# Optimization experiments

Hardware: AMD Instinct MI355X
Metric: run time of the kernel (lower is better)

## Reference

```python
import jax, jax.numpy as jnp
import numpy as np

B, T, C = 4, 1024, 1024
H, G = 16, 1            # n_head, n_query_groups
D = C // H              # head_dim = 64
E, K = 4, 1             # moe_num_experts, moe_k
FF = 4 * C              # ffn/expert hidden = 4096
EPS = 1e-5


def setup_inputs() -> dict:
    key = jax.random.key(0)
    ks = jax.random.split(key, 24)
    w = lambda k, shape: (jax.random.normal(k, shape, jnp.float32) * 0.02)
    return {
        "x": jax.random.normal(ks[0], (B, T, C), jnp.float32),
        # attention (torch Linear weights stored as [in, out])
        "wq": w(ks[1], (C, C)), "wk": w(ks[2], (C, C)), "wv": w(ks[3], (C, C)),
        "wo": w(ks[4], (C, C)), "bo": jnp.zeros((C,), jnp.float32),
        # feedforward
        "ff_w1": w(ks[5], (C, FF)), "ff_b1": jnp.zeros((FF,), jnp.float32),
        "ff_w2": w(ks[6], (FF, C)), "ff_b2": jnp.zeros((C,), jnp.float32),
        # MoE experts (stacked) + gate
        "exp_w1": w(ks[7], (E, C, FF)), "exp_b1": jnp.zeros((E, FF), jnp.float32),
        "exp_w2": w(ks[8], (E, FF, C)), "exp_b2": jnp.zeros((E, C), jnp.float32),
        "gate_w": w(ks[9], (C, E)), "gate_b": jnp.zeros((E,), jnp.float32),
        # layernorms
        "ln1_g": jnp.ones((C,), jnp.float32), "ln1_b": jnp.zeros((C,), jnp.float32),
        "ln2_g": jnp.ones((C,), jnp.float32), "ln2_b": jnp.zeros((C,), jnp.float32),
        "ln3_g": jnp.ones((C,), jnp.float32), "ln3_b": jnp.zeros((C,), jnp.float32),
    }


def _ln(x, g, b):
    m = x.mean(-1, keepdims=True)
    v = x.var(-1, keepdims=True)
    return (x - m) / jnp.sqrt(v + EPS) * g + b


def reference(x, wq, wk, wv, wo, bo, ff_w1, ff_b1, ff_w2, ff_b2,
              exp_w1, exp_b1, exp_w2, exp_b2, gate_w, gate_b,
              ln1_g, ln1_b, ln2_g, ln2_b, ln3_g, ln3_b):
    Hg = H // G
    # ---- grouped-query causal self-attention ----
    h = _ln(x, ln1_g, ln1_b)
    # [B,T,C] -> [B,G,Hg,T,D]
    q = (h @ wq).reshape(B, T, G, Hg, D).transpose(0, 2, 3, 1, 4)
    k = (h @ wk).reshape(B, T, G, Hg, D).transpose(0, 2, 3, 1, 4)
    v = (h @ wv).reshape(B, T, G, Hg, D).transpose(0, 2, 3, 1, 4)
    scores = jnp.einsum('bghtd,bghsd->bghts', q, k) / np.float32(np.sqrt(D))
    causal = jnp.tril(jnp.ones((T, T), bool))
    scores = jnp.where(causal, scores, -jnp.inf)
    probs = jax.nn.softmax(scores, axis=-1)
    o = jnp.einsum('bghts,bghsd->bghtd', probs, v)          # [B,G,Hg,T,D]
    o = o.reshape(B, H, T, D).transpose(0, 2, 1, 3).reshape(B, T, C)
    x = x + o @ wo + bo
    # ---- dense feedforward ----
    h = _ln(x, ln2_g, ln2_b)
    x = x + jax.nn.relu(h @ ff_w1 + ff_b1) @ ff_w2 + ff_b2
    # ---- MoE: compute ALL experts densely, gather top-k (faithful to source) ----
    h = _ln(x, ln3_g, ln3_b)
    gate = h @ gate_w + gate_b                               # [B,T,E]
    topk_s, topk_i = jax.lax.top_k(gate, K)                  # [B,T,K]
    topk_w = jax.nn.softmax(topk_s, axis=-1)
    hidden = jax.nn.relu(jnp.einsum('btc,ech->bteh', h, exp_w1) + exp_b1)
    expert_out = jnp.einsum('bteh,ehc->btec', hidden, exp_w2) + exp_b2  # [B,T,E,C]
    sel = jnp.take_along_axis(expert_out, topk_i[..., None], axis=2)    # [B,T,K,C]
    moe = (sel * topk_w[..., None]).sum(axis=2)
    return x + moe
```

## Files before the change

### kernel.cpp

```cpp
#include <hip/hip_runtime.h>


using f16   = _Float16;
using f16x4 = __attribute__((ext_vector_type(4))) _Float16;
using f16x8 = __attribute__((ext_vector_type(8))) _Float16;
using f32x4 = __attribute__((ext_vector_type(4))) float;

__device__ __forceinline__ void async16(void* l, const void* g) {
  __builtin_amdgcn_global_load_lds(
      (const __attribute__((address_space(1))) unsigned*)g,
      (__attribute__((address_space(3))) unsigned*)l, 16, 0, 0);
}

template <bool SPLITW>
__global__ __launch_bounds__(256) void transpose_k(
    const float* __restrict__ in, f16* __restrict__ oh, f16* __restrict__ ol,
    int R, int Cc) {
  __shared__ float tile[32][33];
  const int nbx = Cc >> 5;
  const int bx = blockIdx.x % nbx, by = blockIdx.x / nbx;
  const int tx = threadIdx.x & 31, ty = threadIdx.x >> 5;
#pragma unroll
  for (int i = 0; i < 4; ++i) {
    int r = ty + i * 8;
    tile[r][tx] = in[(size_t)(by * 32 + r) * Cc + bx * 32 + tx];
  }
  __syncthreads();
#pragma unroll
  for (int i = 0; i < 4; ++i) {
    int oc = ty + i * 8;
    float v = tile[tx][oc];
    size_t o = (size_t)(bx * 32 + oc) * R + by * 32 + tx;
    f16 hi = (f16)v;
    oh[o] = hi;
    if constexpr (SPLITW) ol[o] = (f16)(v - (float)hi);
  }
}

__global__ __launch_bounds__(256) void ln_k(
    const float* __restrict__ x, const float* __restrict__ g,
    const float* __restrict__ b, f16* __restrict__ outh, f16* __restrict__ outl) {
  const int row = blockIdx.x;
  const float4 vv = ((const float4*)(x + (size_t)row * 1024))[threadIdx.x];
  float s = vv.x + vv.y + vv.z + vv.w;
  float sq = vv.x * vv.x + vv.y * vv.y + vv.z * vv.z + vv.w * vv.w;
#pragma unroll
  for (int mm = 32; mm; mm >>= 1) { s += __shfl_xor(s, mm); sq += __shfl_xor(sq, mm); }
  __shared__ float red[8];
  const int wv = threadIdx.x >> 6;
  if ((threadIdx.x & 63) == 0) { red[wv] = s; red[4 + wv] = sq; }
  __syncthreads();
  s = red[0] + red[1] + red[2] + red[3];
  sq = red[4] + red[5] + red[6] + red[7];
  const float mean = s * 0.0009765625f;
  const float rstd = rsqrtf(sq * 0.0009765625f - mean * mean + 1e-5f);
  const int c = threadIdx.x * 4;
  const float xs[4] = {vv.x, vv.y, vv.z, vv.w};
  f16x4 ovh, ovl;
#pragma unroll
  for (int i = 0; i < 4; ++i) {
    float val = (xs[i] - mean) * rstd * g[c + i] + b[c + i];
    f16 hi = (f16)val;
    ovh[i] = hi;
    ovl[i] = (f16)(val - (float)hi);
  }
  *(f16x4*)(outh + (size_t)row * 1024 + c) = ovh;
  *(f16x4*)(outl + (size_t)row * 1024 + c) = ovl;
}

__global__ __launch_bounds__(256) void gate_k(
    const float* __restrict__ x, const float* __restrict__ g, const float* __restrict__ b,
    const float* __restrict__ gw, const float* __restrict__ gb,
    int* __restrict__ cnt, int* __restrict__ idxAll) {
  const int t = blockIdx.x;
  const float4 vv = ((const float4*)(x + (size_t)t * 1024))[threadIdx.x];
  float s = vv.x + vv.y + vv.z + vv.w;
  float sq = vv.x * vv.x + vv.y * vv.y + vv.z * vv.z + vv.w * vv.w;
#pragma unroll
  for (int mm = 32; mm; mm >>= 1) { s += __shfl_xor(s, mm); sq += __shfl_xor(sq, mm); }
  __shared__ float red[8];
  __shared__ float redv[4][4];
  const int wv = threadIdx.x >> 6;
  if ((threadIdx.x & 63) == 0) { red[wv] = s; red[4 + wv] = sq; }
  __syncthreads();
  s = red[0] + red[1] + red[2] + red[3];
  sq = red[4] + red[5] + red[6] + red[7];
  const float mean = s * 0.0009765625f;
  const float rstd = rsqrtf(sq * 0.0009765625f - mean * mean + 1e-5f);
  const int c = threadIdx.x * 4;
  const float xs[4] = {vv.x, vv.y, vv.z, vv.w};
  float a0 = 0.f, a1 = 0.f, a2 = 0.f, a3 = 0.f;
#pragma unroll
  for (int i = 0; i < 4; ++i) {
    float ln = (xs[i] - mean) * rstd * g[c + i] + b[c + i];
    const float4 w4 = ((const float4*)gw)[c + i];
    a0 += ln * w4.x; a1 += ln * w4.y; a2 += ln * w4.z; a3 += ln * w4.w;
  }
#pragma unroll
  for (int mm = 32; mm; mm >>= 1) {
    a0 += __shfl_xor(a0, mm); a1 += __shfl_xor(a1, mm);
    a2 += __shfl_xor(a2, mm); a3 += __shfl_xor(a3, mm);
  }
  if ((threadIdx.x & 63) == 0) {
    redv[wv][0] = a0; redv[wv][1] = a1; redv[wv][2] = a2; redv[wv][3] = a3;
  }
  __syncthreads();
  if (threadIdx.x == 0) {
    float ge[4];
#pragma unroll
    for (int e = 0; e < 4; ++e)
      ge[e] = redv[0][e] + redv[1][e] + redv[2][e] + redv[3][e] + gb[e];
    int be = 0; float bvv = ge[0];
#pragma unroll
    for (int e = 1; e < 4; ++e) if (ge[e] > bvv) { bvv = ge[e]; be = e; }
    int pos = atomicAdd(&cnt[be], 1);
    idxAll[(be << 12) + pos] = t;
  }
}

__global__ void init_moe(int* cnt) { if (threadIdx.x < 4) cnt[threadIdx.x] = 0; }

template <bool SPLIT, bool RELU, bool BIAS, bool RES, bool GATHER, int OUT, bool QKV3>
__global__ __launch_bounds__(256, 2) void gemm_k(
    const f16* __restrict__ Ah, const f16* __restrict__ Al,
    const f16* __restrict__ Bh, const f16* __restrict__ Bl,
    float* __restrict__ outf, f16* __restrict__ outh, f16* __restrict__ outl,
    const float* __restrict__ bias, const float* __restrict__ res,
    const int* __restrict__ idxAll, const int* __restrict__ cntAll,
    int M, int N, int K) {
  const int NB = N >> 7;
  int bid = blockIdx.x;
  int cnt = M;
  const int* idx = nullptr;
  if constexpr (GATHER) {
    const int MBNB = 32 * NB;
    int e = bid / MBNB; bid -= e * MBNB;
    cnt = cntAll[e];
    idx = idxAll + (e << 12);
    Bh += (size_t)e * N * K;
    if (BIAS) bias += (size_t)e * N;
  }
  const int m0 = (bid / NB) << 7, n0 = (bid % NB) << 7;
  if (GATHER && m0 >= cnt) return;

  __shared__ __align__(16) char lds[65536];

  const int tid = threadIdx.x;
  const int wave = tid >> 6, lane = tid & 63;
  const int wr = (wave >> 1) << 6, wc = (wave & 1) << 6;
  const int lc = (lane & 7) ^ (lane >> 3);
  const int srow = lane >> 3;

  const char* srcA[4];
  const char* srcB[4];
  const int kofs = (SPLIT ? (lc >> 1) : lc) * 16;
#pragma unroll
  for (int s = 0; s < 4; ++s) {
    const int tr = (wave * 4 + s) * 8 + srow;
    int gm = m0 + tr;
    if constexpr (GATHER) gm = idx[gm < cnt ? gm : cnt - 1];
    const f16* baseA = (SPLIT && (lc & 1)) ? Al : Ah;
    srcA[s] = (const char*)baseA + ((size_t)gm * K) * 2 + kofs;
    const f16* baseB = (SPLIT && (lc & 1)) ? Bl : Bh;
    srcB[s] = (const char*)baseB + ((size_t)(n0 + tr) * K) * 2 + kofs;
  }
  char* const ldsw = lds + wave * 4096;

  const int s4 = lane >> 4, l7 = lane & 7, fr = lane & 15;
  int offAh[4], offAl[4], offBh[4], offBl[4];
#pragma unroll
  for (int i = 0; i < 4; ++i) {
    const int row = wr + i * 16 + fr;
    const int col = wc + i * 16 + fr;
    if constexpr (SPLIT) {
      offAh[i] = row * 128 + (((2 * s4) ^ l7) << 4);
      offAl[i] = row * 128 + (((2 * s4 + 1) ^ l7) << 4);
      offBh[i] = 16384 + col * 128 + (((2 * s4) ^ l7) << 4);
      offBl[i] = 16384 + col * 128 + (((2 * s4 + 1) ^ l7) << 4);
    } else {
      offAh[i] = row * 128 + ((s4 ^ l7) << 4);
      offAl[i] = row * 128 + (((4 + s4) ^ l7) << 4);
      offBh[i] = 16384 + col * 128 + ((s4 ^ l7) << 4);
      offBl[i] = 16384 + col * 128 + (((4 + s4) ^ l7) << 4);
    }
  }

  f32x4 acc[4][4] = {};

  constexpr int KSTEP = SPLIT ? 32 : 64;
  const int nt = K / KSTEP;

#pragma unroll
  for (int s = 0; s < 4; ++s) {
    async16(ldsw + s * 1024, srcA[s]);
    async16(ldsw + 16384 + s * 1024, srcB[s]);
  }

  for (int t = 0; t < nt; ++t) {
    const int cur = t & 1;
    if (t + 1 < nt) {
      const size_t kb = (size_t)(t + 1) * (KSTEP * 2);
      char* dst = ldsw + (cur ^ 1) * 32768;
#pragma unroll
      for (int s = 0; s < 4; ++s) {
        async16(dst + s * 1024, srcA[s] + kb);
        async16(dst + 16384 + s * 1024, srcB[s] + kb);
      }
      asm volatile("s_waitcnt vmcnt(8)" ::: "memory");
    } else {
      asm volatile("s_waitcnt vmcnt(0)" ::: "memory");
    }
    __builtin_amdgcn_s_barrier();
    __builtin_amdgcn_sched_barrier(0);

    const char* cab = lds + cur * 32768;
    f16x8 va[4], vb[4], va2[4], vb2[4];
#pragma unroll
    for (int i = 0; i < 4; ++i) {
      va[i]  = *(const f16x8*)(cab + offAh[i]);
      va2[i] = *(const f16x8*)(cab + offAl[i]);
      vb[i]  = *(const f16x8*)(cab + offBh[i]);
      vb2[i] = *(const f16x8*)(cab + offBl[i]);
    }
    __builtin_amdgcn_s_setprio(1);
#pragma unroll
    for (int i = 0; i < 4; ++i)
#pragma unroll
      for (int j = 0; j < 4; ++j) {
        if constexpr (SPLIT) {
          acc[i][j] = __builtin_amdgcn_mfma_f32_16x16x32_f16(va[i],  vb[j],  acc[i][j], 0, 0, 0);
          acc[i][j] = __builtin_amdgcn_mfma_f32_16x16x32_f16(va2[i], vb[j],  acc[i][j], 0, 0, 0);
          acc[i][j] = __builtin_amdgcn_mfma_f32_16x16x32_f16(va[i],  vb2[j], acc[i][j], 0, 0, 0);
        } else {
          acc[i][j] = __builtin_amdgcn_mfma_f32_16x16x32_f16(va[i],  vb[j],  acc[i][j], 0, 0, 0);
          acc[i][j] = __builtin_amdgcn_mfma_f32_16x16x32_f16(va2[i], vb2[j], acc[i][j], 0, 0, 0);
        }
      }
    __builtin_amdgcn_s_setprio(0);
    __builtin_amdgcn_sched_barrier(0);
    __builtin_amdgcn_s_barrier();
  }

  const int cl = lane & 15, rg = lane >> 4;
#pragma unroll
  for (int i = 0; i < 4; ++i) {
#pragma unroll
    for (int r = 0; r < 4; ++r) {
      const int mloc = m0 + wr + i * 16 + rg * 4 + r;
      if (GATHER && mloc >= cnt) continue;
      const int orow = GATHER ? idx[mloc] : mloc;
#pragma unroll
      for (int j = 0; j < 4; ++j) {
        const int col = n0 + wc + j * 16 + cl;
        float v2 = acc[i][j][r];
        if (BIAS) v2 += bias[col];
        if (RELU) v2 = v2 > 0.f ? v2 : 0.f;
        if (RES) v2 += res[(size_t)orow * N + col];
        size_t oidx;
        if constexpr (QKV3) oidx = ((size_t)(col >> 10) * M + orow) * 1024 + (col & 1023);
        else oidx = (size_t)orow * N + col;
        if constexpr (OUT == 0) {
          outf[oidx] = v2;
        } else if constexpr (OUT == 1) {
          f16 hi = (f16)v2;
          outh[oidx] = hi;
          outl[oidx] = (f16)(v2 - (float)hi);
        } else {
          outh[oidx] = (f16)v2;
        }
      }
    }
  }
}

__global__ __launch_bounds__(256, 2) void attn_k(
    const f16* __restrict__ qh, const f16* __restrict__ ql,
    const f16* __restrict__ kh, const f16* __restrict__ kl,
    const f16* __restrict__ vh, const f16* __restrict__ vl,
    f16* __restrict__ oh, f16* __restrict__ ol) {
  const int qt = blockIdx.x & 15, hd = (blockIdx.x >> 4) & 15, bb = blockIdx.x >> 8;
  const int tid = threadIdx.x, wave = tid >> 6, lane = tid & 63;
  __shared__ __align__(16) char Qs[16384], Ks[16384], Vs[16384], Ps[16384];
  const int swz = (((lane & 7) ^ ((lane >> 3) & 7)) << 4);
  const size_t tok0 = (size_t)bb * 1024;
  const int hoff = hd * 64;
  const float L2E = 1.44269504089f;

#pragma unroll
  for (int r = 0; r < 2; ++r) {
    const int chunk = wave * 2 + r;
    const int row = chunk * 8 + (lane >> 3);
    const size_t byte = (((tok0 + qt * 64 + row) * 1024 + hoff) << 1) + swz;
    async16(Qs + chunk * 1024, (const char*)qh + byte);
    async16(Qs + 8192 + chunk * 1024, (const char*)ql + byte);
  }

  f32x4 oacc[4] = {};
  float mrun[4] = {-1e30f, -1e30f, -1e30f, -1e30f};
  float lrun[4] = {};

  for (int kt = 0; kt <= qt; ++kt) {
    __syncthreads();
#pragma unroll
    for (int r = 0; r < 2; ++r) {
      const int chunk = wave * 2 + r;
      const int row = chunk * 8 + (lane >> 3);
      const size_t byte = (((tok0 + kt * 64 + row) * 1024 + hoff) << 1) + swz;
      async16(Ks + chunk * 1024, (const char*)kh + byte);
      async16(Ks + 8192 + chunk * 1024, (const char*)kl + byte);
    }
    {
      const int kv = tid >> 2, d0 = (tid & 3) << 4;
      const size_t vbase = (tok0 + kt * 64 + kv) * 1024 + hoff + d0;
      f16x8 a0 = *(const f16x8*)(vh + vbase);
      f16x8 a1 = *(const f16x8*)(vh + vbase + 8);
      f16x8 c0 = *(const f16x8*)(vl + vbase);
      f16x8 c1 = *(const f16x8*)(vl + vbase + 8);
#pragma unroll
      for (int jj = 0; jj < 8; ++jj) {
        const int d = d0 + jj, d2 = d0 + 8 + jj;
        const int o1 = d * 128 + ((kv * 2) ^ ((d & 7) << 4));
        const int o2 = d2 * 128 + ((kv * 2) ^ ((d2 & 7) << 4));
        *(f16*)(Vs + o1) = a0[jj]; *(f16*)(Vs + 8192 + o1) = c0[jj];
        *(f16*)(Vs + o2) = a1[jj]; *(f16*)(Vs + 8192 + o2) = c1[jj];
      }
    }
    __syncthreads();

    f32x4 s[4] = {};
#pragma unroll
    for (int ks = 0; ks < 2; ++ks) {
      const int qrow = wave * 16 + (lane & 15);
      const int qoff = qrow * 128 + ((((ks << 2) + (lane >> 4)) ^ (qrow & 7)) << 4);
      f16x8 a_h = *(const f16x8*)(Qs + qoff);
      f16x8 a_l = *(const f16x8*)(Qs + 8192 + qoff);
#pragma unroll
      for (int j = 0; j < 4; ++j) {
        const int col = j * 16 + (lane & 15);
        const int koff = col * 128 + ((((ks << 2) + (lane >> 4)) ^ (col & 7)) << 4);
        f16x8 b_h = *(const f16x8*)(Ks + koff);
        f16x8 b_l = *(const f16x8*)(Ks + 8192 + koff);
        s[j] = __builtin_amdgcn_mfma_f32_16x16x32_f16(a_h, b_h, s[j], 0, 0, 0);
        s[j] = __builtin_amdgcn_mfma_f32_16x16x32_f16(a_l, b_h, s[j], 0, 0, 0);
        s[j] = __builtin_amdgcn_mfma_f32_16x16x32_f16(a_h, b_l, s[j], 0, 0, 0);
      }
    }

    const bool diag = (kt == qt);
    float pmax[4] = {-1e30f, -1e30f, -1e30f, -1e30f};
#pragma unroll
    for (int j = 0; j < 4; ++j)
#pragma unroll
      for (int r = 0; r < 4; ++r) {
        float sv = s[j][r] * 0.125f;
        if (diag) {
          const int qloc = wave * 16 + (lane >> 4) * 4 + r;
          const int kvl = j * 16 + (lane & 15);
          if (kvl > qloc) sv = -1e30f;
        }
        s[j][r] = sv;
        pmax[r] = fmaxf(pmax[r], sv);
      }
    char* pbh = Ps + wave * 2048;
    char* pbl = Ps + 8192 + wave * 2048;
#pragma unroll
    for (int r = 0; r < 4; ++r) {
#pragma unroll
      for (int mm = 1; mm < 16; mm <<= 1)
        pmax[r] = fmaxf(pmax[r], __shfl_xor(pmax[r], mm, 16));
      const float mnew = fmaxf(mrun[r], pmax[r]);
      const float al = exp2f((mrun[r] - mnew) * L2E);
      mrun[r] = mnew;
      lrun[r] *= al;
      oacc[0][r] *= al; oacc[1][r] *= al; oacc[2][r] *= al; oacc[3][r] *= al;
    }

    float psum[4] = {};
#pragma unroll
    for (int j = 0; j < 4; ++j)
#pragma unroll
      for (int r = 0; r < 4; ++r) {
        const float p = exp2f((s[j][r] - mrun[r]) * L2E);
        psum[r] += p;
        const int lr = (lane >> 4) * 4 + r;
        const int kvl = j * 16 + (lane & 15);
        const int poff = lr * 128 + ((kvl * 2) ^ ((lr & 7) << 4));
        f16 ph = (f16)p;
        *(f16*)(pbh + poff) = ph;
        *(f16*)(pbl + poff) = (f16)(p - (float)ph);
      }
#pragma unroll
    for (int r = 0; r < 4; ++r) {
#pragma unroll
      for (int mm = 1; mm < 16; mm <<= 1)
        psum[r] += __shfl_xor(psum[r], mm, 16);
      lrun[r] += psum[r];
    }

#pragma unroll
    for (int ks = 0; ks < 2; ++ks) {
      const int prow = lane & 15;
      const int poff = prow * 128 + ((((ks << 2) + (lane >> 4)) ^ (prow & 7)) << 4);
      f16x8 a_h = *(const f16x8*)(pbh + poff);
      f16x8 a_l = *(const f16x8*)(pbl + poff);
#pragma unroll
      for (int jd = 0; jd < 4; ++jd) {
        const int col = jd * 16 + (lane & 15);
        const int voff = col * 128 + ((((ks << 2) + (lane >> 4)) ^ (col & 7)) << 4);
        f16x8 b_h = *(const f16x8*)(Vs + voff);
        f16x8 b_l = *(const f16x8*)(Vs + 8192 + voff);
        oacc[jd] = __builtin_amdgcn_mfma_f32_16x16x32_f16(a_h, b_h, oacc[jd], 0, 0, 0);
        oacc[jd] = __builtin_amdgcn_mfma_f32_16x16x32_f16(a_l, b_h, oacc[jd], 0, 0, 0);
        oacc[jd] = __builtin_amdgcn_mfma_f32_16x16x32_f16(a_h, b_l, oacc[jd], 0, 0, 0);
      }
    }
  }

#pragma unroll
  for (int r = 0; r < 4; ++r) {
    const float inv = 1.0f / lrun[r];
    const size_t trow = tok0 + qt * 64 + wave * 16 + (lane >> 4) * 4 + r;
#pragma unroll
    for (int jd = 0; jd < 4; ++jd) {
      const int col = hoff + jd * 16 + (lane & 15);
      const float val = oacc[jd][r] * inv;
      const f16 hi = (f16)val;
      oh[trow * 1024 + col] = hi;
      ol[trow * 1024 + col] = (f16)(val - (float)hi);
    }
  }
}

extern "C" void kernel_launch(void* const* d_in, const int* in_sizes, int n_in,
                              void* d_out, int out_size, void* d_ws, size_t ws_size,
                              hipStream_t stream) {
  const float* x0   = (const float*)d_in[0];
  const float* wq   = (const float*)d_in[1];
  const float* wk   = (const float*)d_in[2];
  const float* wv   = (const float*)d_in[3];
  const float* wo   = (const float*)d_in[4];
  const float* bo   = (const float*)d_in[5];
  const float* ffw1 = (const float*)d_in[6];
  const float* ffb1 = (const float*)d_in[7];
  const float* ffw2 = (const float*)d_in[8];
  const float* ffb2 = (const float*)d_in[9];
  const float* ew1  = (const float*)d_in[10];
  const float* eb1  = (const float*)d_in[11];
  const float* ew2  = (const float*)d_in[12];
  const float* eb2  = (const float*)d_in[13];
  const float* gw   = (const float*)d_in[14];
  const float* gb   = (const float*)d_in[15];
  const float* l1g  = (const float*)d_in[16];
  const float* l1b  = (const float*)d_in[17];
  const float* l2g  = (const float*)d_in[18];
  const float* l2b  = (const float*)d_in[19];
  const float* l3g  = (const float*)d_in[20];
  const float* l3b  = (const float*)d_in[21];
  float* out = (float*)d_out;

  char* w = (char*)d_ws;
  const size_t M1 = (size_t)1024 * 1024;
  const size_t A1 = (size_t)4096 * 1024 * 2;
  const size_t W4 = (size_t)1024 * 4096 * 2;
  f16* wqkvh = (f16*)w; w += 3 * M1 * 2;
  f16* wqkvl = (f16*)w; w += 3 * M1 * 2;
  f16* woh = (f16*)w; w += M1 * 2;  f16* wol = (f16*)w; w += M1 * 2;
  f16* f1h = (f16*)w; w += W4;  f16* f1l = (f16*)w; w += W4;
  f16* f2h = (f16*)w; w += W4;  f16* f2l = (f16*)w; w += W4;
  f16* e1t = (f16*)w; w += 4 * W4;
  f16* e2t = (f16*)w; w += 4 * W4;
  f16* hh  = (f16*)w; w += A1;  f16* hl  = (f16*)w; w += A1;
  f16* qkv_h = (f16*)w; w += 3 * A1;
  f16* qkv_l = (f16*)w; w += 3 * A1;
  f16* o_h = (f16*)w; w += A1;  f16* o_l = (f16*)w; w += A1;
  float* x1 = (float*)w; w += (size_t)4096 * 1024 * 4;
  int* cnt = (int*)w; w += 256;
  int* idx = (int*)w; w += (size_t)4 * 4096 * 4;
  f16* hid_h = qkv_h;
  f16* hid_l = (f16*)((char*)qkv_h + (size_t)32 * 1024 * 1024);
  f16* ffh   = qkv_h;

  transpose_k<true><<<1024, 256, 0, stream>>>(wq, wqkvh, wqkvl, 1024, 1024);
  transpose_k<true><<<1024, 256, 0, stream>>>(wk, wqkvh + M1, wqkvl + M1, 1024, 1024);
  transpose_k<true><<<1024, 256, 0, stream>>>(wv, wqkvh + 2 * M1, wqkvl + 2 * M1, 1024, 1024);
  transpose_k<true><<<1024, 256, 0, stream>>>(wo, woh, wol, 1024, 1024);
  transpose_k<true><<<4096, 256, 0, stream>>>(ffw1, f1h, f1l, 1024, 4096);
  transpose_k<true><<<4096, 256, 0, stream>>>(ffw2, f2h, f2l, 4096, 1024);
  for (int e = 0; e < 4; ++e) {
    transpose_k<false><<<4096, 256, 0, stream>>>(
        ew1 + (size_t)e * 1024 * 4096, e1t + (size_t)e * 4096 * 1024, nullptr, 1024, 4096);
    transpose_k<false><<<4096, 256, 0, stream>>>(
        ew2 + (size_t)e * 4096 * 1024, e2t + (size_t)e * 1024 * 4096, nullptr, 4096, 1024);
  }

  const size_t TOK = (size_t)4096 * 1024;
  ln_k<<<4096, 256, 0, stream>>>(x0, l1g, l1b, hh, hl);
  gemm_k<true, false, false, false, false, 1, true><<<768, 256, 0, stream>>>(
      hh, hl, wqkvh, wqkvl, nullptr, qkv_h, qkv_l, nullptr, nullptr, nullptr, nullptr,
      4096, 3072, 1024);
  attn_k<<<1024, 256, 0, stream>>>(qkv_h, qkv_l, qkv_h + TOK, qkv_l + TOK,
                                   qkv_h + 2 * TOK, qkv_l + 2 * TOK, o_h, o_l);
  gemm_k<true, false, true, true, false, 0, false><<<256, 256, 0, stream>>>(
      o_h, o_l, woh, wol, x1, nullptr, nullptr, bo, x0, nullptr, nullptr, 4096, 1024, 1024);

  ln_k<<<4096, 256, 0, stream>>>(x1, l2g, l2b, hh, hl);
  gemm_k<true, true, true, false, false, 1, false><<<1024, 256, 0, stream>>>(
      hh, hl, f1h, f1l, nullptr, hid_h, hid_l, ffb1, nullptr, nullptr, nullptr,
      4096, 4096, 1024);
  gemm_k<true, false, true, true, false, 0, false><<<256, 256, 0, stream>>>(
      hid_h, hid_l, f2h, f2l, out, nullptr, nullptr, ffb2, x1, nullptr, nullptr,
      4096, 1024, 4096);

  ln_k<<<4096, 256, 0, stream>>>(out, l3g, l3b, hh, hl);
  init_moe<<<1, 64, 0, stream>>>(cnt);
  gate_k<<<4096, 256, 0, stream>>>(out, l3g, l3b, gw, gb, cnt, idx);
  gemm_k<false, true, true, false, true, 2, false><<<4096, 256, 0, stream>>>(
      hh, nullptr, e1t, nullptr, nullptr, ffh, nullptr, eb1, nullptr, idx, cnt,
      4096, 4096, 1024);
  gemm_k<false, false, true, true, true, 0, false><<<1024, 256, 0, stream>>>(
      ffh, nullptr, e2t, nullptr, out, nullptr, nullptr, eb2, out, idx, cnt,
      4096, 1024, 4096);
}
```

Baseline: 808.3 us.

## Use 8-wave GEMM blocks with triple-buffered LDS and block-id swizzle

The GEMM kernel moves from 4 waves to 8 waves per 128x128 tile, so each wave now computes a 64x32 sub-tile. LDS staging becomes three buffers instead of two, letting two K-tiles be prefetched ahead of compute. Block indices are also remapped with a stride-8 swizzle, which changes which tiles run together and may improve L2 reuse. The cost is 96KB of LDS per block, which may limit how many blocks fit per CU, plus extra barrier traffic across more waves.

Result: slower. 1.165 ms (+44.1%).

```diff
diff --git a/kernel.cpp b/kernel.cpp
--- a/kernel.cpp
+++ b/kernel.cpp
@@ -121,7 +121,7 @@
 __global__ void init_moe(int* cnt) { if (threadIdx.x < 4) cnt[threadIdx.x] = 0; }
 
 template <bool SPLIT, bool RELU, bool BIAS, bool RES, bool GATHER, int OUT, bool QKV3>
-__global__ __launch_bounds__(256, 2) void gemm_k(
+__global__ __launch_bounds__(512, 2) void gemm_k(
     const f16* __restrict__ Ah, const f16* __restrict__ Al,
     const f16* __restrict__ Bh, const f16* __restrict__ Bl,
     float* __restrict__ outf, f16* __restrict__ outh, f16* __restrict__ outl,
@@ -129,34 +129,40 @@
     const int* __restrict__ idxAll, const int* __restrict__ cntAll,
     int M, int N, int K) {
   const int NB = N >> 7;
-  int bid = blockIdx.x;
+  int bid;
   int cnt = M;
   const int* idx = nullptr;
   if constexpr (GATHER) {
     const int MBNB = 32 * NB;
-    int e = bid / MBNB; bid -= e * MBNB;
+    const int e = blockIdx.x / MBNB;
+    const int inner = blockIdx.x - e * MBNB;
+    const int q2 = MBNB >> 3;
+    bid = (inner & 7) * q2 + (inner >> 3);
     cnt = cntAll[e];
     idx = idxAll + (e << 12);
     Bh += (size_t)e * N * K;
     if (BIAS) bias += (size_t)e * N;
+  } else {
+    const int q2 = gridDim.x >> 3;
+    bid = ((int)blockIdx.x & 7) * q2 + ((int)blockIdx.x >> 3);
   }
   const int m0 = (bid / NB) << 7, n0 = (bid % NB) << 7;
   if (GATHER && m0 >= cnt) return;
 
-  __shared__ __align__(16) char lds[65536];
+  __shared__ __align__(16) char lds[98304];
 
   const int tid = threadIdx.x;
   const int wave = tid >> 6, lane = tid & 63;
-  const int wr = (wave >> 1) << 6, wc = (wave & 1) << 6;
-  const int lc = (lane & 7) ^ (lane >> 3);
+  const int wr = (wave >> 2) << 6, wc = (wave & 3) << 5;
   const int srow = lane >> 3;
-
-  const char* srcA[4];
-  const char* srcB[4];
-  const int kofs = (SPLIT ? (lc >> 1) : lc) * 16;
-#pragma unroll
-  for (int s = 0; s < 4; ++s) {
-    const int tr = (wave * 4 + s) * 8 + srow;
+  const int lc = (lane & 7) ^ srow;
+  const int kofs = (SPLIT ? (lc >> 1) : lc) << 4;
+
+  const char* srcA[2];
+  const char* srcB[2];
+#pragma unroll
+  for (int s = 0; s < 2; ++s) {
+    const int tr = wave * 16 + s * 8 + srow;
     int gm = m0 + tr;
     if constexpr (GATHER) gm = idx[gm < cnt ? gm : cnt - 1];
     const f16* baseA = (SPLIT && (lc & 1)) ? Al : Ah;
@@ -164,76 +170,78 @@
     const f16* baseB = (SPLIT && (lc & 1)) ? Bl : Bh;
     srcB[s] = (const char*)baseB + ((size_t)(n0 + tr) * K) * 2 + kofs;
   }
-  char* const ldsw = lds + wave * 4096;
 
   const int s4 = lane >> 4, l7 = lane & 7, fr = lane & 15;
-  int offAh[4], offAl[4], offBh[4], offBl[4];
+  const int c0 = (SPLIT ? (2 * s4) : s4) ^ l7;
+  const int c1 = (SPLIT ? (2 * s4 + 1) : (4 + s4)) ^ l7;
+  int offA[4][2], offB[2][2];
 #pragma unroll
   for (int i = 0; i < 4; ++i) {
     const int row = wr + i * 16 + fr;
-    const int col = wc + i * 16 + fr;
-    if constexpr (SPLIT) {
-      offAh[i] = row * 128 + (((2 * s4) ^ l7) << 4);
-      offAl[i] = row * 128 + (((2 * s4 + 1) ^ l7) << 4);
-      offBh[i] = 16384 + col * 128 + (((2 * s4) ^ l7) << 4);
-      offBl[i] = 16384 + col * 128 + (((2 * s4 + 1) ^ l7) << 4);
-    } else {
-      offAh[i] = row * 128 + ((s4 ^ l7) << 4);
-      offAl[i] = row * 128 + (((4 + s4) ^ l7) << 4);
-      offBh[i] = 16384 + col * 128 + ((s4 ^ l7) << 4);
-      offBl[i] = 16384 + col * 128 + (((4 + s4) ^ l7) << 4);
-    }
-  }
-
-  f32x4 acc[4][4] = {};
+    offA[i][0] = row * 128 + c0 * 16;
+    offA[i][1] = row * 128 + c1 * 16;
+  }
+#pragma unroll
+  for (int j = 0; j < 2; ++j) {
+    const int col = wc + j * 16 + fr;
+    offB[j][0] = 16384 + col * 128 + c0 * 16;
+    offB[j][1] = 16384 + col * 128 + c1 * 16;
+  }
+
+  f32x4 acc[4][2] = {};
 
   constexpr int KSTEP = SPLIT ? 32 : 64;
   const int nt = K / KSTEP;
 
-#pragma unroll
-  for (int s = 0; s < 4; ++s) {
-    async16(ldsw + s * 1024, srcA[s]);
-    async16(ldsw + 16384 + s * 1024, srcB[s]);
-  }
+  auto stage = [&](int buf, int tile) {
+    const size_t kb = (size_t)tile * (KSTEP * 2);
+    char* dst = lds + buf * 32768 + wave * 2048;
+    async16(dst, srcA[0] + kb);
+    async16(dst + 1024, srcA[1] + kb);
+    async16(dst + 16384, srcB[0] + kb);
+    async16(dst + 16384 + 1024, srcB[1] + kb);
+  };
+
+  stage(0, 0);
+  stage(1, 1);
 
   for (int t = 0; t < nt; ++t) {
-    const int cur = t & 1;
-    if (t + 1 < nt) {
-      const size_t kb = (size_t)(t + 1) * (KSTEP * 2);
-      char* dst = ldsw + (cur ^ 1) * 32768;
-#pragma unroll
-      for (int s = 0; s < 4; ++s) {
-        async16(dst + s * 1024, srcA[s] + kb);
-        async16(dst + 16384 + s * 1024, srcB[s] + kb);
-      }
+    const int cb = t % 3;
+    if (t + 2 < nt) {
+      stage((t + 2) % 3, t + 2);
       asm volatile("s_waitcnt vmcnt(8)" ::: "memory");
+    } else if (t + 1 < nt) {
+      asm volatile("s_waitcnt vmcnt(4)" ::: "memory");
     } else {
       asm volatile("s_waitcnt vmcnt(0)" ::: "memory");
     }
     __builtin_amdgcn_s_barrier();
     __builtin_amdgcn_sched_barrier(0);
 
-    const char* cab = lds + cur * 32768;
-    f16x8 va[4], vb[4], va2[4], vb2[4];
+    const char* base = lds + cb * 32768;
+    f16x8 va[4][2], vb[2][2];
 #pragma unroll
     for (int i = 0; i < 4; ++i) {
-      va[i]  = *(const f16x8*)(cab + offAh[i]);
-      va2[i] = *(const f16x8*)(cab + offAl[i]);
-      vb[i]  = *(const f16x8*)(cab + offBh[i]);
-      vb2[i] = *(const f16x8*)(cab + offBl[i]);
+      va[i][0] = *(const f16x8*)(base + offA[i][0]);
+      va[i][1] = *(const f16x8*)(base + offA[i][1]);
+    }
+#pragma unroll
+    for (int j = 0; j < 2; ++j) {
+      vb[j][0] = *(const f16x8*)(base + offB[j][0]);
+      vb[j][1] = *(const f16x8*)(base + offB[j][1]);
     }
     __builtin_amdgcn_s_setprio(1);
 #pragma unroll
     for (int i = 0; i < 4; ++i)
 #pragma unroll
-      for (int j = 0; j < 4; ++j) {
+      for (int j = 0; j < 2; ++j) {
         if constexpr (SPLIT) {
-          acc[i][j] = __builtin_amdgcn_mfma_f32_16x16x32_f16(va[i],  vb[j],  acc[i][j], 0, 0, 0);
-          acc[i][j] = __builtin_amdgcn_mfma_f32_16x16x32_f16(va2[i], vb[j],  acc[i][j], 0, 0, 0);
-          acc[i][j] = __builtin_amdgcn_mfma_f32_16x16x32_f16(va[i],  vb2[j], acc[i][j], 0, 0, 0);
+          acc[i][j] = __builtin_amdgcn_mfma_f32_16x16x32_f16(va[i][0], vb[j][0], acc[i][j], 0, 0, 0);
+          acc[i][j] = __builtin_amdgcn_mfma_f32_16x16x32_f16(va[i][1], vb[j][0], acc[i][j], 0, 0, 0);
+          acc[i][j] = __builtin_amdgcn_mfma_f32_16x16x32_f16(va[i][0], vb[j][1], acc[i][j], 0, 0, 0);
         } else {
-          acc[i][j] = __builtin_amdgcn_mfma_f32_16x16x32_f16(va[i],  vb[j],  acc[i][j], 0, 0, 0);
-          acc[i][j] = __builtin_amdgcn_mfma_f32_16x16x32_f16(va2[i], vb2[j], acc[i][j], 0, 0, 0);
+          acc[i][j] = __builtin_amdgcn_mfma_f32_16x16x32_f16(va[i][0], vb[j][0], acc[i][j], 0, 0, 0);
+          acc[i][j] = __builtin_amdgcn_mfma_f32_16x16x32_f16(va[i][1], vb[j][1], acc[i][j], 0, 0, 0);
         }
       }
     __builtin_amdgcn_s_setprio(0);
@@ -250,7 +258,7 @@
       if (GATHER && mloc >= cnt) continue;
       const int orow = GATHER ? idx[mloc] : mloc;
 #pragma unroll
-      for (int j = 0; j < 4; ++j) {
+      for (int j = 0; j < 2; ++j) {
         const int col = n0 + wc + j * 16 + cl;
         float v2 = acc[i][j][r];
         if (BIAS) v2 += bias[col];
@@ -495,29 +503,29 @@
 
   const size_t TOK = (size_t)4096 * 1024;
   ln_k<<<4096, 256, 0, stream>>>(x0, l1g, l1b, hh, hl);
-  gemm_k<true, false, false, false, false, 1, true><<<768, 256, 0, stream>>>(
+  gemm_k<true, false, false, false, false, 1, true><<<768, 512, 0, stream>>>(
       hh, hl, wqkvh, wqkvl, nullptr, qkv_h, qkv_l, nullptr, nullptr, nullptr, nullptr,
       4096, 3072, 1024);
   attn_k<<<1024, 256, 0, stream>>>(qkv_h, qkv_l, qkv_h + TOK, qkv_l + TOK,
                                    qkv_h + 2 * TOK, qkv_l + 2 * TOK, o_h, o_l);
-  gemm_k<true, false, true, true, false, 0, false><<<256, 256, 0, stream>>>(
+  gemm_k<true, false, true, true, false, 0, false><<<256, 512, 0, stream>>>(
       o_h, o_l, woh, wol, x1, nullptr, nullptr, bo, x0, nullptr, nullptr, 4096, 1024, 1024);
 
   ln_k<<<4096, 256, 0, stream>>>(x1, l2g, l2b, hh, hl);
-  gemm_k<true, true, true, false, false, 1, false><<<1024, 256, 0, stream>>>(
+  gemm_k<true, true, true, false, false, 1, false><<<1024, 512, 0, stream>>>(
       hh, hl, f1h, f1l, nullptr, hid_h, hid_l, ffb1, nullptr, nullptr, nullptr,
       4096, 4096, 1024);
-  gemm_k<true, false, true, true, false, 0, false><<<256, 256, 0, stream>>>(
+  gemm_k<true, false, true, true, false, 0, false><<<256, 512, 0, stream>>>(
       hid_h, hid_l, f2h, f2l, out, nullptr, nullptr, ffb2, x1, nullptr, nullptr,
       4096, 1024, 4096);
 
   ln_k<<<4096, 256, 0, stream>>>(out, l3g, l3b, hh, hl);
   init_moe<<<1, 64, 0, stream>>>(cnt);
   gate_k<<<4096, 256, 0, stream>>>(out, l3g, l3b, gw, gb, cnt, idx);
-  gemm_k<false, true, true, false, true, 2, false><<<4096, 256, 0, stream>>>(
+  gemm_k<false, true, true, false, true, 2, false><<<4096, 512, 0, stream>>>(
       hh, nullptr, e1t, nullptr, nullptr, ffh, nullptr, eb1, nullptr, idx, cnt,
       4096, 4096, 1024);
-  gemm_k<false, false, true, true, true, 0, false><<<1024, 256, 0, stream>>>(
+  gemm_k<false, false, true, true, true, 0, false><<<1024, 512, 0, stream>>>(
       ffh, nullptr, e2t, nullptr, out, nullptr, nullptr, eb2, out, idx, cnt,
       4096, 1024, 4096);
 }
```

## Split-K for N=1024 GEMMs with separate bias/residual reduce kernel

Applied to the files above, without the earlier changes.

The three GEMMs with N=1024 (attention output projection, FFN down-projection, MoE expert down-projection) now split K in half. This doubles the number of blocks, which then write two fp32 partial buffers. A new reduce kernel sums the partials and adds bias and residual; for MoE it picks the per-token expert bias through an expert-id array recorded by the gate kernel. A block-index swizzle is also added to regroup tile order. The aim is to fill more of the GPU's CUs on under-occupied launches, at the cost of extra partial-buffer memory traffic and additional kernel launches, with scratch buffers aliased onto workspace regions that are dead at that point.

New measurement: 954.3 us. 18.1% more time.

```diff
diff --git a/kernel.cpp b/kernel.cpp
--- a/kernel.cpp
+++ b/kernel.cpp
@@ -71,7 +71,7 @@
 __global__ __launch_bounds__(256) void gate_k(
     const float* __restrict__ x, const float* __restrict__ g, const float* __restrict__ b,
     const float* __restrict__ gw, const float* __restrict__ gb,
-    int* __restrict__ cnt, int* __restrict__ idxAll) {
+    int* __restrict__ cnt, int* __restrict__ idxAll, int* __restrict__ eid) {
   const int t = blockIdx.x;
   const float4 vv = ((const float4*)(x + (size_t)t * 1024))[threadIdx.x];
   float s = vv.x + vv.y + vv.z + vv.w;
@@ -115,30 +115,63 @@
     for (int e = 1; e < 4; ++e) if (ge[e] > bvv) { bvv = ge[e]; be = e; }
     int pos = atomicAdd(&cnt[be], 1);
     idxAll[(be << 12) + pos] = t;
+    eid[t] = be;
   }
 }
 
 __global__ void init_moe(int* cnt) { if (threadIdx.x < 4) cnt[threadIdx.x] = 0; }
 
-template <bool SPLIT, bool RELU, bool BIAS, bool RES, bool GATHER, int OUT, bool QKV3>
+template <bool MOE>
+__global__ __launch_bounds__(256) void reduce_k(
+    const float* __restrict__ p0, const float* __restrict__ p1,
+    const float* __restrict__ res, const float* __restrict__ bias,
+    const int* __restrict__ eid, float* __restrict__ o) {
+  const int row = blockIdx.x, t = threadIdx.x;
+  const float* bp = MOE ? bias + (size_t)eid[row] * 1024 : bias;
+  const float4 a = ((const float4*)(p0 + (size_t)row * 1024))[t];
+  const float4 b = ((const float4*)(p1 + (size_t)row * 1024))[t];
+  const float4 r = ((const float4*)(res + (size_t)row * 1024))[t];
+  const float4 bb = ((const float4*)bp)[t];
+  float4 o4;
+  o4.x = r.x + a.x + b.x + bb.x;
+  o4.y = r.y + a.y + b.y + bb.y;
+  o4.z = r.z + a.z + b.z + bb.z;
+  o4.w = r.w + a.w + b.w + bb.w;
+  ((float4*)(o + (size_t)row * 1024))[t] = o4;
+}
+
+template <bool SPLIT, bool RELU, bool BIAS, bool RES, bool GATHER, int OUT,
+          bool QKV3, bool KSPLIT>
 __global__ __launch_bounds__(256, 2) void gemm_k(
     const f16* __restrict__ Ah, const f16* __restrict__ Al,
     const f16* __restrict__ Bh, const f16* __restrict__ Bl,
-    float* __restrict__ outf, f16* __restrict__ outh, f16* __restrict__ outl,
+    float* __restrict__ outf, float* __restrict__ outf2,
+    f16* __restrict__ outh, f16* __restrict__ outl,
     const float* __restrict__ bias, const float* __restrict__ res,
     const int* __restrict__ idxAll, const int* __restrict__ cntAll,
     int M, int N, int K) {
   const int NB = N >> 7;
-  int bid = blockIdx.x;
+  int bid, ks = 0;
   int cnt = M;
   const int* idx = nullptr;
   if constexpr (GATHER) {
     const int MBNB = 32 * NB;
-    int e = bid / MBNB; bid -= e * MBNB;
+    const int per = KSPLIT ? 2 * MBNB : MBNB;
+    const int e = blockIdx.x / per;
+    int rem = blockIdx.x - e * per;
+    if constexpr (KSPLIT) { ks = rem >= MBNB; rem -= ks * MBNB; }
+    const int q2 = MBNB >> 3;
+    bid = (rem & 7) * q2 + (rem >> 3);
     cnt = cntAll[e];
     idx = idxAll + (e << 12);
     Bh += (size_t)e * N * K;
     if (BIAS) bias += (size_t)e * N;
+  } else {
+    int rem = blockIdx.x;
+    const int ntile = (int)gridDim.x >> (KSPLIT ? 1 : 0);
+    if constexpr (KSPLIT) { ks = rem >= ntile; rem -= ks * ntile; }
+    const int q2 = ntile >> 3;
+    bid = (rem & 7) * q2 + (rem >> 3);
   }
   const int m0 = (bid / NB) << 7, n0 = (bid % NB) << 7;
   if (GATHER && m0 >= cnt) return;
@@ -148,21 +181,23 @@
   const int tid = threadIdx.x;
   const int wave = tid >> 6, lane = tid & 63;
   const int wr = (wave >> 1) << 6, wc = (wave & 1) << 6;
-  const int lc = (lane & 7) ^ (lane >> 3);
   const int srow = lane >> 3;
+  const int lc = (lane & 7) ^ srow;
+  const int kofs = (SPLIT ? (lc >> 1) : lc) << 4;
+
+  const int kshift = (KSPLIT && ks) ? (K >> 1) : 0;
 
   const char* srcA[4];
   const char* srcB[4];
-  const int kofs = (SPLIT ? (lc >> 1) : lc) * 16;
 #pragma unroll
   for (int s = 0; s < 4; ++s) {
     const int tr = (wave * 4 + s) * 8 + srow;
     int gm = m0 + tr;
     if constexpr (GATHER) gm = idx[gm < cnt ? gm : cnt - 1];
     const f16* baseA = (SPLIT && (lc & 1)) ? Al : Ah;
-    srcA[s] = (const char*)baseA + ((size_t)gm * K) * 2 + kofs;
+    srcA[s] = (const char*)baseA + ((size_t)gm * K + kshift) * 2 + kofs;
     const f16* baseB = (SPLIT && (lc & 1)) ? Bl : Bh;
-    srcB[s] = (const char*)baseB + ((size_t)(n0 + tr) * K) * 2 + kofs;
+    srcB[s] = (const char*)baseB + ((size_t)(n0 + tr) * K + kshift) * 2 + kofs;
   }
   char* const ldsw = lds + wave * 4096;
 
@@ -188,7 +223,7 @@
   f32x4 acc[4][4] = {};
 
   constexpr int KSTEP = SPLIT ? 32 : 64;
-  const int nt = K / KSTEP;
+  const int nt = (KSPLIT ? (K >> 1) : K) / KSTEP;
 
 #pragma unroll
   for (int s = 0; s < 4; ++s) {
@@ -242,6 +277,7 @@
   }
 
   const int cl = lane & 15, rg = lane >> 4;
+  float* const po = (OUT == 3) ? (ks ? outf2 : outf) : outf;
 #pragma unroll
   for (int i = 0; i < 4; ++i) {
 #pragma unroll
@@ -259,8 +295,8 @@
         size_t oidx;
         if constexpr (QKV3) oidx = ((size_t)(col >> 10) * M + orow) * 1024 + (col & 1023);
         else oidx = (size_t)orow * N + col;
-        if constexpr (OUT == 0) {
-          outf[oidx] = v2;
+        if constexpr (OUT == 0 || OUT == 3) {
+          po[oidx] = v2;
         } else if constexpr (OUT == 1) {
           f16 hi = (f16)v2;
           outh[oidx] = hi;
@@ -464,7 +500,8 @@
   const size_t W4 = (size_t)1024 * 4096 * 2;
   f16* wqkvh = (f16*)w; w += 3 * M1 * 2;
   f16* wqkvl = (f16*)w; w += 3 * M1 * 2;
-  f16* woh = (f16*)w; w += M1 * 2;  f16* wol = (f16*)w; w += M1 * 2;
+  f16* woh = (f16*)w; w += M1 * 2;
+  f16* wol = (f16*)w; w += M1 * 2;
   f16* f1h = (f16*)w; w += W4;  f16* f1l = (f16*)w; w += W4;
   f16* f2h = (f16*)w; w += W4;  f16* f2l = (f16*)w; w += W4;
   f16* e1t = (f16*)w; w += 4 * W4;
@@ -476,9 +513,16 @@
   float* x1 = (float*)w; w += (size_t)4096 * 1024 * 4;
   int* cnt = (int*)w; w += 256;
   int* idx = (int*)w; w += (size_t)4 * 4096 * 4;
+  int* eid = (int*)w; w += (size_t)4096 * 4;
   f16* hid_h = qkv_h;
-  f16* hid_l = (f16*)((char*)qkv_h + (size_t)32 * 1024 * 1024);
+  f16* hid_l = (f16*)((char*)qkv_h + (((size_t)32) << 20));
   f16* ffh   = qkv_h;
+  float* pW0 = (float*)hh;
+  float* pW1 = (float*)qkv_h;
+  float* pF0 = (float*)wqkvh;
+  float* pF1 = (float*)hh;
+  float* pM0 = (float*)((char*)qkv_l + (((size_t)8) << 20));
+  float* pM1 = (float*)o_h;
 
   transpose_k<true><<<1024, 256, 0, stream>>>(wq, wqkvh, wqkvl, 1024, 1024);
   transpose_k<true><<<1024, 256, 0, stream>>>(wk, wqkvh + M1, wqkvl + M1, 1024, 1024);
@@ -495,29 +539,33 @@
 
   const size_t TOK = (size_t)4096 * 1024;
   ln_k<<<4096, 256, 0, stream>>>(x0, l1g, l1b, hh, hl);
-  gemm_k<true, false, false, false, false, 1, true><<<768, 256, 0, stream>>>(
-      hh, hl, wqkvh, wqkvl, nullptr, qkv_h, qkv_l, nullptr, nullptr, nullptr, nullptr,
-      4096, 3072, 1024);
+  gemm_k<true, false, false, false, false, 1, true, false><<<768, 256, 0, stream>>>(
+      hh, hl, wqkvh, wqkvl, nullptr, nullptr, qkv_h, qkv_l,
+      nullptr, nullptr, nullptr, nullptr, 4096, 3072, 1024);
   attn_k<<<1024, 256, 0, stream>>>(qkv_h, qkv_l, qkv_h + TOK, qkv_l + TOK,
                                    qkv_h + 2 * TOK, qkv_l + 2 * TOK, o_h, o_l);
-  gemm_k<true, false, true, true, false, 0, false><<<256, 256, 0, stream>>>(
-      o_h, o_l, woh, wol, x1, nullptr, nullptr, bo, x0, nullptr, nullptr, 4096, 1024, 1024);
+  gemm_k<true, false, false, false, false, 3, false, true><<<512, 256, 0, stream>>>(
+      o_h, o_l, woh, wol, pW0, pW1, nullptr, nullptr,
+      nullptr, nullptr, nullptr, nullptr, 4096, 1024, 1024);
+  reduce_k<false><<<4096, 256, 0, stream>>>(pW0, pW1, x0, bo, nullptr, x1);
 
   ln_k<<<4096, 256, 0, stream>>>(x1, l2g, l2b, hh, hl);
-  gemm_k<true, true, true, false, false, 1, false><<<1024, 256, 0, stream>>>(
-      hh, hl, f1h, f1l, nullptr, hid_h, hid_l, ffb1, nullptr, nullptr, nullptr,
-      4096, 4096, 1024);
-  gemm_k<true, false, true, true, false, 0, false><<<256, 256, 0, stream>>>(
-      hid_h, hid_l, f2h, f2l, out, nullptr, nullptr, ffb2, x1, nullptr, nullptr,
-      4096, 1024, 4096);
+  gemm_k<true, true, true, false, false, 1, false, false><<<1024, 256, 0, stream>>>(
+      hh, hl, f1h, f1l, nullptr, nullptr, hid_h, hid_l,
+      ffb1, nullptr, nullptr, nullptr, 4096, 4096, 1024);
+  gemm_k<true, false, false, false, false, 3, false, true><<<512, 256, 0, stream>>>(
+      hid_h, hid_l, f2h, f2l, pF0, pF1, nullptr, nullptr,
+      nullptr, nullptr, nullptr, nullptr, 4096, 1024, 4096);
+  reduce_k<false><<<4096, 256, 0, stream>>>(pF0, pF1, x1, ffb2, nullptr, out);
 
   ln_k<<<4096, 256, 0, stream>>>(out, l3g, l3b, hh, hl);
   init_moe<<<1, 64, 0, stream>>>(cnt);
-  gate_k<<<4096, 256, 0, stream>>>(out, l3g, l3b, gw, gb, cnt, idx);
-  gemm_k<false, true, true, false, true, 2, false><<<4096, 256, 0, stream>>>(
-      hh, nullptr, e1t, nullptr, nullptr, ffh, nullptr, eb1, nullptr, idx, cnt,
-      4096, 4096, 1024);
-  gemm_k<false, false, true, true, true, 0, false><<<1024, 256, 0, stream>>>(
-      ffh, nullptr, e2t, nullptr, out, nullptr, nullptr, eb2, out, idx, cnt,
-      4096, 1024, 4096);
-}
+  gate_k<<<4096, 256, 0, stream>>>(out, l3g, l3b, gw, gb, cnt, idx, eid);
+  gemm_k<false, true, true, false, true, 2, false, false><<<4096, 256, 0, stream>>>(
+      hh, nullptr, e1t, nullptr, nullptr, nullptr, ffh, nullptr,
+      eb1, nullptr, idx, cnt, 4096, 4096, 1024);
+  gemm_k<false, false, false, false, true, 3, false, true><<<2048, 256, 0, stream>>>(
+      ffh, nullptr, e2t, nullptr, pM0, pM1, nullptr, nullptr,
+      nullptr, nullptr, idx, cnt, 4096, 1024, 4096);
+  reduce_k<true><<<4096, 256, 0, stream>>>(pM0, pM1, out, eb2, eid, out);
+}
```
